# Kernel optimization log

Hardware: AMD Instinct MI355X
Metric: run time of the kernel (lower is better)

## Reference

```python
import jax, jax.numpy as jnp
import numpy as np

K = 20      # self.k in OurModel
TAU = 1.0   # self.tau in OurModel


def _knn_feats(emb, idx, yctx):
    # emb: [N, E] embedding table; idx: [B] int query ids; yctx: [B, N] residual context
    a = emb[idx]                                            # [B, E] gathered query embeddings
    # squared euclidean via gram trick, then sqrt == torch.cdist(p=2)
    d2 = (jnp.sum(a * a, axis=-1, keepdims=True)
          + jnp.sum(emb * emb, axis=-1)[None, :]
          - 2.0 * a @ emb.T)                                 # [B, N]
    sim = jnp.sqrt(jnp.clip(d2, 0.0, None)) + 0.001
    rows = jnp.arange(idx.shape[0])
    sim = sim.at[rows, idx].set(0.0)                         # zero self-distance
    w = jnp.exp(-sim / TAU)                                  # [B, N], self weight == 1 (max)
    # top (K+1) weights; drop the largest (the self entry) -> top-K neighbours.
    # Matches torch argsort(w)[:, -(K+1):-1]; downstream ops are order-invariant reductions.
    topw, topi = jax.lax.top_k(w, K + 1)
    topw = topw[:, 1:]                                       # [B, K]
    sel = jnp.take_along_axis(yctx, topi[:, 1:], axis=1)     # [B, K]
    f1 = jnp.sum(topw, axis=1)                               # sum of weights
    f2 = jnp.sum(sel * topw, axis=1) / jnp.sum(topw, axis=1) # weighted mean
    f3 = jnp.std(sel, axis=1, ddof=1)                        # torch.std is unbiased
    return f1, f2, f3


def _forward(emb0, emb1, rctx0, rctx1, idx0, idx1, mean_in, std_in,
             W1, b1, Wm, bm, Ws, bs):
    a1, a2, a3 = _knn_feats(emb0, idx0, rctx0)
    b1_, b2_, b3_ = _knn_feats(emb1, idx1, rctx1)
    # torch.cat(final1 + final2 + final3 + [mean, std]) column order
    feats = jnp.stack([a1, b1_, a2, b2_, a3, b3_, mean_in, std_in], axis=1)  # [B, 8]
    h = jnp.maximum(feats @ W1 + b1, 0.0)                    # [B, 64]
    mean_out = h @ Wm + bm[0]                                # [B]
    std_out = h @ Ws + bs[0]                                 # [B]
    return mean_out, std_out


def setup_inputs() -> dict:
    key = jax.random.key(0)
    ks = jax.random.split(key, 14)
    B, N, E, H = 512, 50000, 16, 64
    return {
        "emb0": jax.random.normal(ks[0], (N, E), jnp.float32),
        "emb1": jax.random.normal(ks[1], (N, E), jnp.float32),
        "rctx0": jax.random.normal(ks[2], (B, N), jnp.float32),
        "rctx1": jax.random.normal(ks[3], (B, N), jnp.float32),
        "idx0": jax.random.randint(ks[4], (B,), 0, N, jnp.int32),
        "idx1": jax.random.randint(ks[5], (B,), 0, N, jnp.int32),
        "mean_in": jax.random.normal(ks[6], (B,), jnp.float32),
        "std_in": jax.random.normal(ks[7], (B,), jnp.float32),
        "W1": jax.random.normal(ks[8], (8, H), jnp.float32) * 0.1,
        "b1": jax.random.normal(ks[9], (H,), jnp.float32) * 0.1,
        "Wm": jax.random.normal(ks[10], (H,), jnp.float32) * 0.1,
        "bm": jax.random.normal(ks[11], (1,), jnp.float32) * 0.1,
        "Ws": jax.random.normal(ks[12], (H,), jnp.float32) * 0.1,
        "bs": jax.random.normal(ks[13], (1,), jnp.float32) * 0.1,
    }


def reference(emb0, emb1, rctx0, rctx1, idx0, idx1, mean_in, std_in,
              W1, b1, Wm, bm, Ws, bs):
    return _forward(emb0, emb1, rctx0, rctx1, idx0, idx1, mean_in, std_in,
                    W1, b1, Wm, bm, Ws, bs)
```

## Files before the change

kernel.cpp:

```cpp
#include <hip/hip_runtime.h>
#include <math.h>

typedef unsigned long long u64;
typedef unsigned int u32;
#define INF64 0xFFFFFFFFFFFFFFFFULL
#define FBIG 3.3e38f
#define KSEL 20
#define QT   32
#define CNK  16
#define CAP  256
#define PREFT 4
#define DEPS 0.5f
#define NTHR 512

typedef __bf16 bf16x8 __attribute__((ext_vector_type(8)));
typedef float  f32x16 __attribute__((ext_vector_type(16)));
typedef unsigned int uint4e __attribute__((ext_vector_type(4)));

static __device__ __forceinline__ u64 umin64(u64 a, u64 b) { return a < b ? a : b; }
static __device__ __forceinline__ u32 asu(float f) { return __builtin_bit_cast(u32, f); }
static __device__ __forceinline__ float trunchi(u32 u) { return __builtin_bit_cast(float, u & 0xffff0000u); }
#define PERM2(a,b) __builtin_amdgcn_perm((a),(b),0x07060302u)
static __device__ __forceinline__ bf16x8 mk8(u32 a, u32 b, u32 c, u32 d) {
    uint4e t = {a, b, c, d};
    return __builtin_bit_cast(bf16x8, t);
}
static __device__ __forceinline__ f32x16 zero16() {
    f32x16 z = {0.f,0.f,0.f,0.f,0.f,0.f,0.f,0.f,0.f,0.f,0.f,0.f,0.f,0.f,0.f,0.f};
    return z;
}

static __device__ __forceinline__ float dot16(
    float4 a0, float4 a1, float4 a2, float4 a3,
    float4 b0, float4 b1, float4 b2, float4 b3)
{
    float d = 0.f;
    d = fmaf(a0.x, b0.x, d); d = fmaf(a0.y, b0.y, d);
    d = fmaf(a0.z, b0.z, d); d = fmaf(a0.w, b0.w, d);
    d = fmaf(a1.x, b1.x, d); d = fmaf(a1.y, b1.y, d);
    d = fmaf(a1.z, b1.z, d); d = fmaf(a1.w, b1.w, d);
    d = fmaf(a2.x, b2.x, d); d = fmaf(a2.y, b2.y, d);
    d = fmaf(a2.z, b2.z, d); d = fmaf(a2.w, b2.w, d);
    d = fmaf(a3.x, b3.x, d); d = fmaf(a3.y, b3.y, d);
    d = fmaf(a3.z, b3.z, d); d = fmaf(a3.w, b3.w, d);
    return d;
}

static __device__ __forceinline__ void cvt_hilo(float4 f0, float4 f1, bf16x8& hi, bf16x8& lo) {
    u32 u0=asu(f0.x),u1=asu(f0.y),u2=asu(f0.z),u3=asu(f0.w);
    u32 u4=asu(f1.x),u5=asu(f1.y),u6=asu(f1.z),u7=asu(f1.w);
    hi = mk8(PERM2(u1,u0), PERM2(u3,u2), PERM2(u5,u4), PERM2(u7,u6));
    u32 w0=asu(f0.x-trunchi(u0)), w1=asu(f0.y-trunchi(u1));
    u32 w2=asu(f0.z-trunchi(u2)), w3=asu(f0.w-trunchi(u3));
    u32 w4=asu(f1.x-trunchi(u4)), w5=asu(f1.y-trunchi(u5));
    u32 w6=asu(f1.z-trunchi(u6)), w7=asu(f1.w-trunchi(u7));
    lo = mk8(PERM2(w1,w0), PERM2(w3,w2), PERM2(w5,w4), PERM2(w7,w6));
}

static __device__ __forceinline__ f32x16 tile_qe(
    const float* __restrict__ embS, int base, int col, int kb, int N,
    bf16x8 B1, bf16x8 B2)
{
    int row = base + col;
    row = min(row, N - 1);
    const float4* ep = (const float4*)(embS + (size_t)row * 16 + kb * 8);
    float4 f0 = ep[0], f1 = ep[1];
    bf16x8 A1, A2;
    cvt_hilo(f0, f1, A1, A2);
    f32x16 acc = zero16();
    acc = __builtin_amdgcn_mfma_f32_32x32x16_bf16(A1, B1, acc, 0, 0, 0);
    acc = __builtin_amdgcn_mfma_f32_32x32x16_bf16(A1, B2, acc, 0, 0, 0);
    acc = __builtin_amdgcn_mfma_f32_32x32x16_bf16(A2, B1, acc, 0, 0, 0);
    return acc;
}

__global__ __launch_bounds__(256) void norm_kernel(
    const float* __restrict__ emb0, const float* __restrict__ emb1,
    float* __restrict__ neBuf, int N, int npad)
{
    const int j = blockIdx.x * 256 + threadIdx.x;
    const float* __restrict__ e = blockIdx.y ? emb1 : emb0;
    float* __restrict__ o = neBuf + (size_t)blockIdx.y * npad;
    float v = FBIG;
    if (j < N) {
        const float4* p = (const float4*)(e + (size_t)j * 16);
        float4 e0=p[0],e1=p[1],e2=p[2],e3=p[3];
        v = dot16(e0,e1,e2,e3, e0,e1,e2,e3);
    }
    if (j < npad) o[j] = v;
}

__global__ __launch_bounds__(NTHR, 4) void knn_scan_kernel(
    const float* __restrict__ emb0, const float* __restrict__ emb1,
    const int* __restrict__ idx0, const int* __restrict__ idx1,
    const float* __restrict__ neBuf,
    u64* __restrict__ chunkTop, int N, int B, int chlen)
{
    const int tid  = threadIdx.x;
    const int lane = tid & 63;
    const int wv   = tid >> 6;
    const int col  = lane & 31;
    const int kb   = lane >> 5;
    const int bx   = blockIdx.x;
    const int xcd  = bx & 7;
    const int s    = xcd & 1;
    const int t_   = (bx >> 3) * 4 + (xcd >> 1);
    const int c    = t_ & (CNK - 1);
    const int qt   = t_ >> 4;
    const int qbase = qt * QT;
    const int jbeg = c * chlen;
    const int tpc  = chlen >> 5;
    const int npad = chlen * CNK;

    const float* __restrict__ embS = s ? emb1 : emb0;
    const int*   __restrict__ idxp = s ? idx1 : idx0;
    const float* __restrict__ neS  = neBuf + (size_t)s * npad;

    __shared__ float Qs[QT][16];
    __shared__ float naS[QT];
    __shared__ int   sq[QT];
    __shared__ int   scnt[QT];
    __shared__ float sthr[QT];
    __shared__ float sMin[QT][32];
    __shared__ u32   sbuf[QT][CAP];

    if (tid < QT) { sq[tid] = idxp[qbase + tid]; scnt[tid] = 0; }
    __syncthreads();
    if (tid < 128) {
        int q = tid >> 2, part = tid & 3;
        ((float4*)(&Qs[q][0]))[part] = ((const float4*)(embS + (size_t)sq[q] * 16))[part];
    }
    __syncthreads();
    if (tid < QT) {
        const float4* qp = (const float4*)(&Qs[tid][0]);
        float4 a0=qp[0],a1=qp[1],a2=qp[2],a3=qp[3];
        naS[tid] = dot16(a0,a1,a2,a3, a0,a1,a2,a3);
    }
    bf16x8 B1, B2;
    {
        const float4* qp = (const float4*)(&Qs[col][kb * 8]);
        float4 f0 = qp[0], f1 = qp[1];
        cvt_hilo(f0, f1, B1, B2);
    }
    __syncthreads();

    const float na_l  = naS[col];
    const int   self_l = sq[col];

    float m0v = FBIG, m1v = FBIG;
#define PINS(r, nef) { float v_ = fmaf(acc[r], -2.f, na_l + (nef)); \
    float t1_ = fminf(m1v, fmaxf(m0v, v_)); m0v = fminf(m0v, v_); m1v = t1_; }
    for (int pt = 0; pt < PREFT; ++pt) {
        const int t = wv + pt * 8;
        const int base = jbeg + t * 32;
        const float4* np_ = (const float4*)(neS + base + kb * 4);
        float4 n0 = np_[0], n1 = np_[2], n2 = np_[4], n3 = np_[6];
        f32x16 acc = tile_qe(embS, base, col, kb, N, B1, B2);
        PINS(0,n0.x)  PINS(1,n0.y)  PINS(2,n0.z)  PINS(3,n0.w)
        PINS(4,n1.x)  PINS(5,n1.y)  PINS(6,n1.z)  PINS(7,n1.w)
        PINS(8,n2.x)  PINS(9,n2.y)  PINS(10,n2.z) PINS(11,n2.w)
        PINS(12,n3.x) PINS(13,n3.y) PINS(14,n3.z) PINS(15,n3.w)
    }
#undef PINS
    sMin[col][(wv * 2 + kb) * 2 + 0] = m0v;
    sMin[col][(wv * 2 + kb) * 2 + 1] = m1v;
    __syncthreads();

    for (int qq = 0; qq < 4; ++qq) {
        const int q = wv * 4 + qq;
        float v = (lane < 32) ? sMin[q][lane] : FBIG;
        float gm = 0.f;
        for (int r = 0; r < KSEL + 1; ++r) {
            float cm = v;
#pragma unroll
            for (int o = 32; o; o >>= 1) cm = fminf(cm, __shfl_xor(cm, o, 64));
            gm = cm;
            if (v == gm) v = FBIG;
        }
        if (lane == 0) sthr[q] = gm + DEPS;
    }
    __syncthreads();
    const float thr_l = sthr[col];

#define EPI(r, nef) { float ad_ = fmaf(acc[r], -2.f, na_l + (nef)); \
    if (ad_ <= thr_l) msk |= (1u << (r)); }
    for (int t = wv; t < tpc; t += 8) {
        const int base = jbeg + t * 32;
        const float4* np_ = (const float4*)(neS + base + kb * 4);
        float4 n0 = np_[0], n1 = np_[2], n2 = np_[4], n3 = np_[6];
        f32x16 acc = tile_qe(embS, base, col, kb, N, B1, B2);
        u32 msk = 0;
        EPI(0,n0.x)  EPI(1,n0.y)  EPI(2,n0.z)  EPI(3,n0.w)
        EPI(4,n1.x)  EPI(5,n1.y)  EPI(6,n1.z)  EPI(7,n1.w)
        EPI(8,n2.x)  EPI(9,n2.y)  EPI(10,n2.z) EPI(11,n2.w)
        EPI(12,n3.x) EPI(13,n3.y) EPI(14,n3.z) EPI(15,n3.w)
        if (msk) {
#pragma unroll
            for (int r = 0; r < 16; ++r) if (msk & (1u << r)) {
                int j = base + (r & 3) + 8 * (r >> 2) + 4 * kb;
                if (j != self_l) {
                    int sl = atomicAdd(&scnt[col], 1);
                    if (sl < CAP) sbuf[col][sl] = (u32)j;
                }
            }
        }
    }
#undef EPI
    __syncthreads();

    for (int qq = 0; qq < 4; ++qq) {
        const int q = wv * 4 + qq;
        const int M = min(scnt[q], CAP);
        const float4* qp = (const float4*)(&Qs[q][0]);
        const float4 q0=qp[0], q1=qp[1], q2=qp[2], q3=qp[3];
        const float naq = naS[q];
        auto rk = [&](int i) -> u64 {
            int j = (int)sbuf[q][i];
            const float4* p = (const float4*)(embS + (size_t)j * 16);
            float4 e0=p[0],e1=p[1],e2=p[2],e3=p[3];
            float ne_ = dot16(e0,e1,e2,e3, e0,e1,e2,e3);
            float qe  = dot16(q0,q1,q2,q3, e0,e1,e2,e3);
            float dd  = fmaxf(fmaf(qe, -2.f, naq + ne_), 0.f);
            return ((u64)asu(dd) << 32) | (u32)j;
        };
        u64 k0 = INF64, k1 = INF64, k2 = INF64, k3 = INF64;
        if (lane < M)       k0 = rk(lane);
        if (lane + 64 < M)  k1 = rk(lane + 64);
        if (lane + 128 < M) k2 = rk(lane + 128);
        if (lane + 192 < M) k3 = rk(lane + 192);
        u64 keep = INF64;
        if (M <= 128) {
            for (int r = 0; r < KSEL; ++r) {
                u64 cm = umin64(k0, k1);
#pragma unroll
                for (int o = 32; o; o >>= 1) cm = umin64(cm, __shfl_xor(cm, o, 64));
                if (k0 == cm) k0 = INF64;
                if (k1 == cm) k1 = INF64;
                if (lane == r) keep = cm;
            }
        } else {
            for (int r = 0; r < KSEL; ++r) {
                u64 cm = umin64(umin64(k0, k1), umin64(k2, k3));
#pragma unroll
                for (int o = 32; o; o >>= 1) cm = umin64(cm, __shfl_xor(cm, o, 64));
                if (k0 == cm) k0 = INF64;
                if (k1 == cm) k1 = INF64;
                if (k2 == cm) k2 = INF64;
                if (k3 == cm) k3 = INF64;
                if (lane == r) keep = cm;
            }
        }
        if (lane < KSEL)
            chunkTop[((size_t)(s * B + qbase + q) * CNK + c) * KSEL + lane] = keep;
    }
}

__global__ __launch_bounds__(128) void merge_mlp_kernel(
    const u64* __restrict__ chunkTop,
    const float* __restrict__ rctx0, const float* __restrict__ rctx1,
    const float* __restrict__ mean_in, const float* __restrict__ std_in,
    const float* __restrict__ W1, const float* __restrict__ b1,
    const float* __restrict__ Wm, const float* __restrict__ bm,
    const float* __restrict__ Ws, const float* __restrict__ bs,
    float* __restrict__ out, int N, int B)
{
    const int b = blockIdx.x;
    const int tid = threadIdx.x;
    const int s = tid >> 6;
    const int lane = tid & 63;
    __shared__ float sf[8];

    const u64* src = chunkTop + ((size_t)(s * B + b)) * (CNK * KSEL);
    u64 v0 = src[lane];
    u64 v1 = src[lane + 64];
    u64 v2 = src[lane + 128];
    u64 v3 = src[lane + 192];
    u64 v4 = src[lane + 256];
    u64 keep = INF64;
    for (int r = 0; r < KSEL; ++r) {
        u64 cm = umin64(umin64(umin64(v0, v1), umin64(v2, v3)), v4);
#pragma unroll
        for (int o = 32; o; o >>= 1) cm = umin64(cm, __shfl_xor(cm, o, 64));
        if (v0 == cm) v0 = INF64;
        if (v1 == cm) v1 = INF64;
        if (v2 == cm) v2 = INF64;
        if (v3 == cm) v3 = INF64;
        if (v4 == cm) v4 = INF64;
        if (lane == r) keep = cm;
    }
    float w = 0.f, sv = 0.f;
    if (lane < KSEL) {
        float d2 = __uint_as_float((unsigned int)(keep >> 32));
        int j = (int)(unsigned int)(keep & 0xFFFFFFFFULL);
        float sim = sqrtf(d2) + 0.001f;
        w = expf(-sim);
        const float* __restrict__ rctx = s ? rctx1 : rctx0;
        sv = rctx[(size_t)b * N + j];
    }
    float sw = w, ssw = sv * w, ss = sv, ss2 = sv * sv;
#pragma unroll
    for (int o = 32; o; o >>= 1) {
        sw  += __shfl_down(sw,  o, 64);
        ssw += __shfl_down(ssw, o, 64);
        ss  += __shfl_down(ss,  o, 64);
        ss2 += __shfl_down(ss2, o, 64);
    }
    if (lane == 0) {
        sf[0 + s] = sw;
        sf[2 + s] = ssw / sw;
        float mean = ss * (1.f / KSEL);
        float var = (ss2 - (float)KSEL * mean * mean) * (1.f / (KSEL - 1));
        sf[4 + s] = sqrtf(fmaxf(var, 0.f));
        if (s == 0) { sf[6] = mean_in[b]; sf[7] = std_in[b]; }
    }
    __syncthreads();

    if (tid < 64) {
        float f0 = sf[0], f1 = sf[1], f2 = sf[2], f3 = sf[3];
        float f4 = sf[4], f5 = sf[5], f6 = sf[6], f7 = sf[7];
        float h = b1[lane];
        h = fmaf(f0, W1[0 * 64 + lane], h);
        h = fmaf(f1, W1[1 * 64 + lane], h);
        h = fmaf(f2, W1[2 * 64 + lane], h);
        h = fmaf(f3, W1[3 * 64 + lane], h);
        h = fmaf(f4, W1[4 * 64 + lane], h);
        h = fmaf(f5, W1[5 * 64 + lane], h);
        h = fmaf(f6, W1[6 * 64 + lane], h);
        h = fmaf(f7, W1[7 * 64 + lane], h);
        h = fmaxf(h, 0.f);
        float mo = h * Wm[lane], so = h * Ws[lane];
#pragma unroll
        for (int o = 32; o; o >>= 1) {
            mo += __shfl_down(mo, o, 64);
            so += __shfl_down(so, o, 64);
        }
        if (lane == 0) {
            out[b] = mo + bm[0];
            out[B + b] = so + bs[0];
        }
    }
}

extern "C" void kernel_launch(void* const* d_in, const int* in_sizes, int n_in,
                              void* d_out, int out_size, void* d_ws, size_t ws_size,
                              hipStream_t stream) {
    const float* emb0    = (const float*)d_in[0];
    const float* emb1    = (const float*)d_in[1];
    const float* rctx0   = (const float*)d_in[2];
    const float* rctx1   = (const float*)d_in[3];
    const int*   idx0    = (const int*)d_in[4];
    const int*   idx1    = (const int*)d_in[5];
    const float* mean_in = (const float*)d_in[6];
    const float* std_in  = (const float*)d_in[7];
    const float* W1      = (const float*)d_in[8];
    const float* b1      = (const float*)d_in[9];
    const float* Wm      = (const float*)d_in[10];
    const float* bm      = (const float*)d_in[11];
    const float* Ws      = (const float*)d_in[12];
    const float* bs      = (const float*)d_in[13];

    const int B = in_sizes[4];
    const int N = in_sizes[0] / 16;

    int chlen = (((N + CNK - 1) / CNK) + 31) & ~31;
    int npad  = chlen * CNK;

    float* neBuf = (float*)d_ws;
    u64* chunkTop = (u64*)((char*)d_ws + (size_t)2 * npad * sizeof(float));

    norm_kernel<<<dim3(npad / 256, 2), 256, 0, stream>>>(emb0, emb1, neBuf, N, npad);

    knn_scan_kernel<<<dim3(2 * (B / QT) * CNK), NTHR, 0, stream>>>(
        emb0, emb1, idx0, idx1, neBuf, chunkTop, N, B, chlen);

    merge_mlp_kernel<<<dim3(B), 128, 0, stream>>>(
        chunkTop, rctx0, rctx1, mean_in, std_in,
        W1, b1, Wm, bm, Ws, bs, (float*)d_out, N, B);
}
```

Before: 311.0 us.

## Replace iterative shuffle-min top-k selection with ballot-based radix threshold search

```diff
diff --git a/kernel.cpp b/kernel.cpp
--- a/kernel.cpp
+++ b/kernel.cpp
@@ -17,7 +17,6 @@
 typedef float  f32x16 __attribute__((ext_vector_type(16)));
 typedef unsigned int uint4e __attribute__((ext_vector_type(4)));
 
-static __device__ __forceinline__ u64 umin64(u64 a, u64 b) { return a < b ? a : b; }
 static __device__ __forceinline__ u32 asu(float f) { return __builtin_bit_cast(u32, f); }
 static __device__ __forceinline__ float trunchi(u32 u) { return __builtin_bit_cast(float, u & 0xffff0000u); }
 #define PERM2(a,b) __builtin_amdgcn_perm((a),(b),0x07060302u)
@@ -162,22 +161,20 @@
         PINS(12,n3.x) PINS(13,n3.y) PINS(14,n3.z) PINS(15,n3.w)
     }
 #undef PINS
-    sMin[col][(wv * 2 + kb) * 2 + 0] = m0v;
-    sMin[col][(wv * 2 + kb) * 2 + 1] = m1v;
+    sMin[col][(wv * 2 + kb) * 2 + 0] = fmaxf(m0v, 0.f);
+    sMin[col][(wv * 2 + kb) * 2 + 1] = fmaxf(m1v, 0.f);
     __syncthreads();
 
     for (int qq = 0; qq < 4; ++qq) {
         const int q = wv * 4 + qq;
-        float v = (lane < 32) ? sMin[q][lane] : FBIG;
-        float gm = 0.f;
-        for (int r = 0; r < KSEL + 1; ++r) {
-            float cm = v;
-#pragma unroll
-            for (int o = 32; o; o >>= 1) cm = fminf(cm, __shfl_xor(cm, o, 64));
-            gm = cm;
-            if (v == gm) v = FBIG;
-        }
-        if (lane == 0) sthr[q] = gm + DEPS;
+        const u32 vb = (lane < 32) ? asu(sMin[q][lane]) : 0xFFFFFFFFu;
+        u32 T = 0;
+        for (int bb = 30; bb >= 0; --bb) {
+            u32 U = T | ((1u << bb) - 1u);
+            int nle = __popcll(__ballot(vb <= U));
+            if (nle < KSEL + 1) T |= (1u << bb);
+        }
+        if (lane == 0) sthr[q] = __uint_as_float(T) + DEPS;
     }
     __syncthreads();
     const float thr_l = sthr[col];
@@ -194,14 +191,13 @@
         EPI(4,n1.x)  EPI(5,n1.y)  EPI(6,n1.z)  EPI(7,n1.w)
         EPI(8,n2.x)  EPI(9,n2.y)  EPI(10,n2.z) EPI(11,n2.w)
         EPI(12,n3.x) EPI(13,n3.y) EPI(14,n3.z) EPI(15,n3.w)
-        if (msk) {
-#pragma unroll
-            for (int r = 0; r < 16; ++r) if (msk & (1u << r)) {
-                int j = base + (r & 3) + 8 * (r >> 2) + 4 * kb;
-                if (j != self_l) {
-                    int sl = atomicAdd(&scnt[col], 1);
-                    if (sl < CAP) sbuf[col][sl] = (u32)j;
-                }
+        while (msk) {
+            int r = __ffs(msk) - 1;
+            msk &= msk - 1;
+            int j = base + (r & 3) + 8 * (r >> 2) + 4 * kb;
+            if (j != self_l) {
+                int sl = atomicAdd(&scnt[col], 1);
+                if (sl < CAP) sbuf[col][sl] = (u32)j;
             }
         }
     }
@@ -218,40 +214,50 @@
             int j = (int)sbuf[q][i];
             const float4* p = (const float4*)(embS + (size_t)j * 16);
             float4 e0=p[0],e1=p[1],e2=p[2],e3=p[3];
-            float ne_ = dot16(e0,e1,e2,e3, e0,e1,e2,e3);
             float qe  = dot16(q0,q1,q2,q3, e0,e1,e2,e3);
-            float dd  = fmaxf(fmaf(qe, -2.f, naq + ne_), 0.f);
+            float dd  = fmaxf(fmaf(qe, -2.f, naq + neS[j]), 0.f);
             return ((u64)asu(dd) << 32) | (u32)j;
         };
-        u64 k0 = INF64, k1 = INF64, k2 = INF64, k3 = INF64;
-        if (lane < M)       k0 = rk(lane);
-        if (lane + 64 < M)  k1 = rk(lane + 64);
-        if (lane + 128 < M) k2 = rk(lane + 128);
-        if (lane + 192 < M) k3 = rk(lane + 192);
-        u64 keep = INF64;
-        if (M <= 128) {
-            for (int r = 0; r < KSEL; ++r) {
-                u64 cm = umin64(k0, k1);
-#pragma unroll
-                for (int o = 32; o; o >>= 1) cm = umin64(cm, __shfl_xor(cm, o, 64));
-                if (k0 == cm) k0 = INF64;
-                if (k1 == cm) k1 = INF64;
-                if (lane == r) keep = cm;
-            }
-        } else {
-            for (int r = 0; r < KSEL; ++r) {
-                u64 cm = umin64(umin64(k0, k1), umin64(k2, k3));
-#pragma unroll
-                for (int o = 32; o; o >>= 1) cm = umin64(cm, __shfl_xor(cm, o, 64));
-                if (k0 == cm) k0 = INF64;
-                if (k1 == cm) k1 = INF64;
-                if (k2 == cm) k2 = INF64;
-                if (k3 == cm) k3 = INF64;
-                if (lane == r) keep = cm;
-            }
-        }
-        if (lane < KSEL)
-            chunkTop[((size_t)(s * B + qbase + q) * CNK + c) * KSEL + lane] = keep;
+        u64 k0 = (lane < M)       ? rk(lane)       : INF64;
+        u64 k1 = (lane + 64 < M)  ? rk(lane + 64)  : INF64;
+        u64 k2 = (lane + 128 < M) ? rk(lane + 128) : INF64;
+        u64 k3 = (lane + 192 < M) ? rk(lane + 192) : INF64;
+        u64 T = 0;
+        for (int bb = 63; bb >= 32; --bb) {
+            u64 U = T | ((1ull << bb) - 1ull);
+            int nle = __popcll(__ballot(k0 <= U)) + __popcll(__ballot(k1 <= U))
+                    + __popcll(__ballot(k2 <= U)) + __popcll(__ballot(k3 <= U));
+            if (nle < KSEL) T |= (1ull << bb);
+        }
+        for (int bb = 15; bb >= 0; --bb) {
+            u64 U = T | ((1ull << bb) - 1ull);
+            int nle = __popcll(__ballot(k0 <= U)) + __popcll(__ballot(k1 <= U))
+                    + __popcll(__ballot(k2 <= U)) + __popcll(__ballot(k3 <= U));
+            if (nle < KSEL) T |= (1ull << bb);
+        }
+        u64* dst = chunkTop + ((size_t)(s * B + qbase + q) * CNK + c) * KSEL;
+        int basec = 0;
+        {
+            u64 mm = __ballot(k0 <= T);
+            if (k0 <= T) { int sl = basec + __popcll(mm & ((1ull << lane) - 1ull)); if (sl < KSEL) dst[sl] = k0; }
+            basec += __popcll(mm);
+        }
+        {
+            u64 mm = __ballot(k1 <= T);
+            if (k1 <= T) { int sl = basec + __popcll(mm & ((1ull << lane) - 1ull)); if (sl < KSEL) dst[sl] = k1; }
+            basec += __popcll(mm);
+        }
+        {
+            u64 mm = __ballot(k2 <= T);
+            if (k2 <= T) { int sl = basec + __popcll(mm & ((1ull << lane) - 1ull)); if (sl < KSEL) dst[sl] = k2; }
+            basec += __popcll(mm);
+        }
+        {
+            u64 mm = __ballot(k3 <= T);
+            if (k3 <= T) { int sl = basec + __popcll(mm & ((1ull << lane) - 1ull)); if (sl < KSEL) dst[sl] = k3; }
+            basec += __popcll(mm);
+        }
+        for (int sl = basec + lane; sl < KSEL; sl += 64) dst[sl] = INF64;
     }
 }
 
@@ -276,28 +282,32 @@
     u64 v2 = src[lane + 128];
     u64 v3 = src[lane + 192];
     u64 v4 = src[lane + 256];
-    u64 keep = INF64;
-    for (int r = 0; r < KSEL; ++r) {
-        u64 cm = umin64(umin64(umin64(v0, v1), umin64(v2, v3)), v4);
-#pragma unroll
-        for (int o = 32; o; o >>= 1) cm = umin64(cm, __shfl_xor(cm, o, 64));
-        if (v0 == cm) v0 = INF64;
-        if (v1 == cm) v1 = INF64;
-        if (v2 == cm) v2 = INF64;
-        if (v3 == cm) v3 = INF64;
-        if (v4 == cm) v4 = INF64;
-        if (lane == r) keep = cm;
-    }
-    float w = 0.f, sv = 0.f;
-    if (lane < KSEL) {
-        float d2 = __uint_as_float((unsigned int)(keep >> 32));
-        int j = (int)(unsigned int)(keep & 0xFFFFFFFFULL);
-        float sim = sqrtf(d2) + 0.001f;
-        w = expf(-sim);
-        const float* __restrict__ rctx = s ? rctx1 : rctx0;
-        sv = rctx[(size_t)b * N + j];
-    }
-    float sw = w, ssw = sv * w, ss = sv, ss2 = sv * sv;
+    u64 T = 0;
+    for (int bb = 63; bb >= 32; --bb) {
+        u64 U = T | ((1ull << bb) - 1ull);
+        int nle = __popcll(__ballot(v0 <= U)) + __popcll(__ballot(v1 <= U))
+                + __popcll(__ballot(v2 <= U)) + __popcll(__ballot(v3 <= U))
+                + __popcll(__ballot(v4 <= U));
+        if (nle < KSEL) T |= (1ull << bb);
+    }
+    for (int bb = 15; bb >= 0; --bb) {
+        u64 U = T | ((1ull << bb) - 1ull);
+        int nle = __popcll(__ballot(v0 <= U)) + __popcll(__ballot(v1 <= U))
+                + __popcll(__ballot(v2 <= U)) + __popcll(__ballot(v3 <= U))
+                + __popcll(__ballot(v4 <= U));
+        if (nle < KSEL) T |= (1ull << bb);
+    }
+    const float* __restrict__ rctx = s ? rctx1 : rctx0;
+    float sw = 0.f, ssw = 0.f, ss = 0.f, ss2 = 0.f;
+#define ACC(vx) if (vx <= T && vx != INF64) { \
+        float d2 = __uint_as_float((u32)((vx) >> 32)); \
+        int j = (int)(u32)((vx) & 0xFFFFFFFFULL); \
+        float sim = sqrtf(d2) + 0.001f; \
+        float wr = expf(-sim); \
+        float svr = rctx[(size_t)b * N + j]; \
+        sw += wr; ssw += svr * wr; ss += svr; ss2 += svr * svr; }
+    ACC(v0) ACC(v1) ACC(v2) ACC(v3) ACC(v4)
+#undef ACC
 #pragma unroll
     for (int o = 32; o; o >>= 1) {
         sw  += __shfl_down(sw,  o, 64);
```

New measurement: 259.5 us. 1.2x faster.
